# Performance work log

Hardware: AMD Instinct MI355X
Metric: run time of the kernel (lower is better)

The kernel has to match this reference:

```python
import jax, jax.numpy as jnp
import numpy as np

L, H, NH, I = 12, 768, 12, 3072
DH = H // NH
EPS = 1e-12
STD = 0.02

def _ln(x, g, b):
    m = jnp.mean(x, axis=-1, keepdims=True)
    v = jnp.mean(jnp.square(x - m), axis=-1, keepdims=True)
    return (x - m) * jax.lax.rsqrt(v + EPS) * g + b

def setup_inputs() -> dict:
    key = jax.random.key(0)
    ks = jax.random.split(key, 6)
    return {
        "hidden_states": jax.random.normal(ks[0], (8, 512, H), dtype=jnp.float32),
        "attention_mask": jnp.zeros((8, 1, 1, 512), dtype=jnp.float32),
        "normA_gamma": jnp.ones((L, H), jnp.float32),
        "normA_beta": jnp.zeros((L, H), jnp.float32),
        "normB_gamma": jnp.ones((L, H), jnp.float32),
        "normB_beta": jnp.zeros((L, H), jnp.float32),
        "wa": jax.random.normal(ks[1], (L, 3 * H, H), jnp.float32) * STD,
        "ba": jnp.zeros((L, 3 * H), jnp.float32),
        "wb": jax.random.normal(ks[2], (L, H, H), jnp.float32) * STD,
        "bb": jnp.zeros((L, H), jnp.float32),
        "wc": jax.random.normal(ks[3], (L, I, H), jnp.float32) * STD,
        "bc": jnp.zeros((L, I), jnp.float32),
        "wd": jax.random.normal(ks[4], (L, H, I), jnp.float32) * STD,
        "bd": jnp.zeros((L, H), jnp.float32),
    }

def _encoder(hidden_states, attention_mask, normA_gamma, normA_beta, normB_gamma,
             normB_beta, wa, ba, wb, bb, wc, bc, wd, bd):
    B, S, _ = hidden_states.shape
    scale = 1.0 / jnp.sqrt(jnp.float32(DH))

    def layer(x, p):
        ga, bA, gB, bB_, Wa, Ba, Wb, Bb, Wc, Bc, Wd, Bd = p
        # fused QKV: [B,S,3H]
        qkv = jnp.einsum('bsh,oh->bso', x, Wa) + Ba
        q, k, v = jnp.split(qkv, 3, axis=-1)
        q = q.reshape(B, S, NH, DH)
        k = k.reshape(B, S, NH, DH)
        v = v.reshape(B, S, NH, DH)
        scores = jnp.einsum('bqnd,bknd->bnqk', q, k) * scale + attention_mask
        probs = jax.nn.softmax(scores, axis=-1)
        ctx = jnp.einsum('bnqk,bknd->bqnd', probs, v).reshape(B, S, H)
        attn_out = jnp.einsum('bsh,oh->bso', ctx, Wb) + Bb
        x = _ln(x + attn_out, ga, bA)           # post-LN after attention
        h = jax.nn.gelu(jnp.einsum('bsh,ih->bsi', x, Wc) + Bc, approximate=False)
        ffn_out = jnp.einsum('bsi,hi->bsh', h, Wd) + Bd
        x = _ln(x + ffn_out, gB, bB_)           # post-LN after FFN
        return x, None

    params = (normA_gamma, normA_beta, normB_gamma, normB_beta,
              wa, ba, wb, bb, wc, bc, wd, bd)
    out, _ = jax.lax.scan(layer, hidden_states, params)
    return out

def reference(hidden_states, attention_mask, normA_gamma, normA_beta, normB_gamma,
              normB_beta, wa, ba, wb, bb, wc, bc, wd, bd):
    return _encoder(hidden_states, attention_mask, normA_gamma, normA_beta,
                    normB_gamma, normB_beta, wa, ba, wb, bb, wc, bc, wd, bd)
```

## Files before the change

kernel.cpp:

```cpp
#include <hip/hip_runtime.h>
#include <hip/hip_bf16.h>
#include <cmath>

typedef __bf16 bf16;
typedef __attribute__((ext_vector_type(8))) __bf16 bf16x8;
typedef __attribute__((ext_vector_type(4))) float f32x4;
typedef __attribute__((ext_vector_type(8))) short s16x8;

#define DEV __device__ __forceinline__

constexpr int HDIM = 768, NHEADS = 12, DHEAD = 64, IDIM = 3072, BATCH = 8, SEQ = 512;
constexpr int MTOK = BATCH * SEQ;
constexpr int H3 = 3 * HDIM;
constexpr float SCALE = 0.125f;

DEV void gld16(const bf16* g, bf16* l) {
  __builtin_amdgcn_global_load_lds((const __attribute__((address_space(1))) void*)g,
                                   (__attribute__((address_space(3))) void*)l, 16, 0, 0);
}

__global__ void k_cvt(const float* __restrict__ s, bf16* __restrict__ o, long n8) {
  long i = (long)blockIdx.x * blockDim.x + threadIdx.x;
  long st = (long)gridDim.x * blockDim.x;
  for (; i < n8; i += st) {
    const float4* p = (const float4*)s + i * 2;
    float4 v0 = p[0], v1 = p[1];
    union { bf16 t[8]; s16x8 v; } u;
    u.t[0] = (bf16)v0.x; u.t[1] = (bf16)v0.y; u.t[2] = (bf16)v0.z; u.t[3] = (bf16)v0.w;
    u.t[4] = (bf16)v1.x; u.t[5] = (bf16)v1.y; u.t[6] = (bf16)v1.z; u.t[7] = (bf16)v1.w;
    *(s16x8*)(o + i * 8) = u.v;
  }
}

__global__ void k_init_xb(const float* __restrict__ s, bf16* __restrict__ xb, long n8) {
  long i = (long)blockIdx.x * blockDim.x + threadIdx.x;
  long st = (long)gridDim.x * blockDim.x;
  for (; i < n8; i += st) {
    const float4* p = (const float4*)s + i * 2;
    float4 v0 = p[0], v1 = p[1];
    union { bf16 t[8]; s16x8 v; } u;
    u.t[0] = (bf16)v0.x; u.t[1] = (bf16)v0.y; u.t[2] = (bf16)v0.z; u.t[3] = (bf16)v0.w;
    u.t[4] = (bf16)v1.x; u.t[5] = (bf16)v1.y; u.t[6] = (bf16)v1.z; u.t[7] = (bf16)v1.w;
    *(s16x8*)(xb + i * 8) = u.v;
  }
}

template <int OUT>
__global__ __launch_bounds__(256) void k_gemm(const bf16* __restrict__ A,
                                              const bf16* __restrict__ W,
                                              const float* __restrict__ bias,
                                              void* __restrict__ C,
                                              bf16* __restrict__ vt,
                                              int M, int N, int K) {
  __shared__ alignas(128) bf16 As[2][128 * 32];
  __shared__ alignas(128) bf16 Bs[2][128 * 32];
  const int tid = threadIdx.x;
  const int lane = tid & 63, wave = tid >> 6;
  const int wr = wave >> 1, wc = wave & 1;
  const int bx = blockIdx.x, by = blockIdx.y;
  const bf16* Ab = A + (size_t)by * 128 * K;
  const bf16* Bb = W + (size_t)bx * 128 * K;
  const int s0 = tid, s1 = tid + 256;
  const int r0 = s0 >> 2, c0 = ((s0 & 3) ^ ((r0 >> 1) & 3)) << 3;
  const int r1 = s1 >> 2, c1 = ((s1 & 3) ^ ((r1 >> 1) & 3)) << 3;

  f32x4 acc[4][4] = {};
  const int KT = K >> 5;
  int cur = 0;
  gld16(Ab + (size_t)r0 * K + c0, &As[0][s0 * 8]);
  gld16(Ab + (size_t)r1 * K + c1, &As[0][s1 * 8]);
  gld16(Bb + (size_t)r0 * K + c0, &Bs[0][s0 * 8]);
  gld16(Bb + (size_t)r1 * K + c1, &Bs[0][s1 * 8]);

  const int r = lane & 15, kg = lane >> 4;
  for (int kt = 0; kt < KT; ++kt) {
    __syncthreads();
    if (kt + 1 < KT) {
      int k0 = (kt + 1) << 5;
      gld16(Ab + (size_t)r0 * K + k0 + c0, &As[cur ^ 1][s0 * 8]);
      gld16(Ab + (size_t)r1 * K + k0 + c1, &As[cur ^ 1][s1 * 8]);
      gld16(Bb + (size_t)r0 * K + k0 + c0, &Bs[cur ^ 1][s0 * 8]);
      gld16(Bb + (size_t)r1 * K + k0 + c1, &Bs[cur ^ 1][s1 * 8]);
    }
    const bf16* Ac = As[cur];
    const bf16* Bc = Bs[cur];
    bf16x8 af[4], bfr[4];
#pragma unroll
    for (int m = 0; m < 4; ++m) {
      int row = wr * 64 + m * 16 + r;
      af[m] = *(const bf16x8*)(Ac + row * 32 + ((kg ^ ((row >> 1) & 3)) << 3));
    }
#pragma unroll
    for (int n = 0; n < 4; ++n) {
      int row = wc * 64 + n * 16 + r;
      bfr[n] = *(const bf16x8*)(Bc + row * 32 + ((kg ^ ((row >> 1) & 3)) << 3));
    }
#pragma unroll
    for (int m = 0; m < 4; ++m)
#pragma unroll
      for (int n = 0; n < 4; ++n)
        acc[m][n] = __builtin_amdgcn_mfma_f32_16x16x32_bf16(af[m], bfr[n], acc[m][n], 0, 0, 0);
    cur ^= 1;
  }
  const int g = lane >> 4, c16 = lane & 15;
#pragma unroll
  for (int m = 0; m < 4; ++m) {
#pragma unroll
    for (int n = 0; n < 4; ++n) {
      int col = bx * 128 + wc * 64 + n * 16 + c16;
      float bv = bias[col];
      if (OUT == 3 && col >= 2 * HDIM) {
        int hh = (col - 2 * HDIM) >> 6, dd = (col - 2 * HDIM) & 63;
        int row0 = by * 128 + wr * 64 + m * 16 + g * 4;
        int bb_ = row0 >> 9, ss = row0 & 511;
        union { bf16 t[4]; short4 q; } u;
#pragma unroll
        for (int j = 0; j < 4; ++j) u.t[j] = (bf16)(acc[m][n][j] + bv);
        *(short4*)(vt + (((size_t)(bb_ * NHEADS + hh) * DHEAD + dd) * SEQ + ss)) = u.q;
      } else {
#pragma unroll
        for (int j = 0; j < 4; ++j) {
          int row = by * 128 + wr * 64 + m * 16 + g * 4 + j;
          float v = acc[m][n][j] + bv;
          if (OUT == 2) v = 0.5f * v * (1.0f + erff(v * 0.70710678118f));
          ((bf16*)C)[(size_t)row * N + col] = (bf16)v;
        }
      }
    }
  }
}

__global__ __launch_bounds__(256) void k_gemm_sk(const bf16* __restrict__ A,
                                                 const bf16* __restrict__ W,
                                                 bf16* __restrict__ C,
                                                 int M, int N, int Kc, int ld) {
  __shared__ alignas(128) bf16 As[2][128 * 32];
  __shared__ alignas(128) bf16 Bs[2][128 * 32];
  const int tid = threadIdx.x;
  const int lane = tid & 63, wave = tid >> 6;
  const int wr = wave >> 1, wc = wave & 1;
  const int bx = blockIdx.x, by = blockIdx.y, kz = blockIdx.z;
  const bf16* Ab = A + (size_t)by * 128 * ld + (size_t)kz * Kc;
  const bf16* Bb = W + (size_t)bx * 128 * ld + (size_t)kz * Kc;
  bf16* Cz = C + (size_t)kz * M * N;
  const int s0 = tid, s1 = tid + 256;
  const int r0 = s0 >> 2, c0 = ((s0 & 3) ^ ((r0 >> 1) & 3)) << 3;
  const int r1 = s1 >> 2, c1 = ((s1 & 3) ^ ((r1 >> 1) & 3)) << 3;

  f32x4 acc[4][4] = {};
  const int KT = Kc >> 5;
  int cur = 0;
  gld16(Ab + (size_t)r0 * ld + c0, &As[0][s0 * 8]);
  gld16(Ab + (size_t)r1 * ld + c1, &As[0][s1 * 8]);
  gld16(Bb + (size_t)r0 * ld + c0, &Bs[0][s0 * 8]);
  gld16(Bb + (size_t)r1 * ld + c1, &Bs[0][s1 * 8]);

  const int r = lane & 15, kg = lane >> 4;
  for (int kt = 0; kt < KT; ++kt) {
    __syncthreads();
    if (kt + 1 < KT) {
      int k0 = (kt + 1) << 5;
      gld16(Ab + (size_t)r0 * ld + k0 + c0, &As[cur ^ 1][s0 * 8]);
      gld16(Ab + (size_t)r1 * ld + k0 + c1, &As[cur ^ 1][s1 * 8]);
      gld16(Bb + (size_t)r0 * ld + k0 + c0, &Bs[cur ^ 1][s0 * 8]);
      gld16(Bb + (size_t)r1 * ld + k0 + c1, &Bs[cur ^ 1][s1 * 8]);
    }
    const bf16* Ac = As[cur];
    const bf16* Bc = Bs[cur];
    bf16x8 af[4], bfr[4];
#pragma unroll
    for (int m = 0; m < 4; ++m) {
      int row = wr * 64 + m * 16 + r;
      af[m] = *(const bf16x8*)(Ac + row * 32 + ((kg ^ ((row >> 1) & 3)) << 3));
    }
#pragma unroll
    for (int n = 0; n < 4; ++n) {
      int row = wc * 64 + n * 16 + r;
      bfr[n] = *(const bf16x8*)(Bc + row * 32 + ((kg ^ ((row >> 1) & 3)) << 3));
    }
#pragma unroll
    for (int m = 0; m < 4; ++m)
#pragma unroll
      for (int n = 0; n < 4; ++n)
        acc[m][n] = __builtin_amdgcn_mfma_f32_16x16x32_bf16(af[m], bfr[n], acc[m][n], 0, 0, 0);
    cur ^= 1;
  }
  const int g = lane >> 4, c16 = lane & 15;
#pragma unroll
  for (int m = 0; m < 4; ++m)
#pragma unroll
    for (int n = 0; n < 4; ++n) {
      int col = bx * 128 + wc * 64 + n * 16 + c16;
#pragma unroll
      for (int j = 0; j < 4; ++j) {
        int row = by * 128 + wr * 64 + m * 16 + g * 4 + j;
        Cz[(size_t)row * N + col] = (bf16)acc[m][n][j];
      }
    }
}

__global__ __launch_bounds__(256) void k_attn(const bf16* __restrict__ qkv,
                                              const bf16* __restrict__ vT,
                                              const float* __restrict__ mask,
                                              bf16* __restrict__ ctx) {
  __shared__ alignas(128) bf16 smem[20480];
  bf16* Qs = smem;
  bf16* Ks = smem + 4096;
  bf16* Vs = smem;
  bf16* Ps = smem + 16384;
  const int tid = threadIdx.x, lane = tid & 63, wave = tid >> 6;
  const int q0 = blockIdx.x * 64;
  const int h = blockIdx.y, b = blockIdx.z;
  const int bh = b * NHEADS + h;
  const bf16* qbase = qkv + (size_t)(b * SEQ) * H3 + h * DHEAD;
  const bf16* kbase = qbase + HDIM;
  const bf16* Vsrc = vT + (size_t)bh * DHEAD * SEQ;
  const int r15 = lane & 15, kg = lane >> 4;

  for (int s = tid; s < 512; s += 256) {
    int r = s >> 3, sl = s & 7;
    gld16(qbase + (size_t)(q0 + r) * H3 + ((sl ^ (r & 7)) << 3), &Qs[s * 8]);
  }
  f32x4 acc[32];
#pragma unroll
  for (int f = 0; f < 32; ++f) acc[f] = (f32x4){0.f, 0.f, 0.f, 0.f};

  for (int half = 0; half < 2; ++half) {
    for (int s = tid; s < 2048; s += 256) {
      int r = s >> 3, sl = s & 7;
      gld16(kbase + (size_t)(half * 256 + r) * H3 + ((sl ^ (r & 7)) << 3), &Ks[s * 8]);
    }
    __syncthreads();
#pragma unroll
    for (int ks = 0; ks < 2; ++ks) {
      int qrow = wave * 16 + r15;
      int sl = ks * 4 + kg;
      bf16x8 aq = *(const bf16x8*)(Qs + qrow * 64 + ((sl ^ (qrow & 7)) << 3));
#pragma unroll
      for (int nf = 0; nf < 16; ++nf) {
        int krow = nf * 16 + r15;
        bf16x8 bk = *(const bf16x8*)(Ks + krow * 64 + ((sl ^ (krow & 7)) << 3));
        acc[half * 16 + nf] =
            __builtin_amdgcn_mfma_f32_16x16x32_bf16(aq, bk, acc[half * 16 + nf], 0, 0, 0);
      }
    }
    __syncthreads();
  }

#pragma unroll
  for (int i = 0; i < 8; ++i) {
    int g16 = tid + i * 256;
    int d = g16 >> 5, c = g16 & 31;
    gld16(Vsrc + (size_t)d * SEQ + ((c ^ (d & 7)) << 3), &Vs[g16 * 8]);
  }

  const float* mrow = mask + b * SEQ;
#pragma unroll
  for (int f = 0; f < 32; ++f) {
    float mv = mrow[f * 16 + r15];
#pragma unroll
    for (int j = 0; j < 4; ++j) acc[f][j] = acc[f][j] * SCALE + mv;
  }
#pragma unroll
  for (int j = 0; j < 4; ++j) {
    float m = -1e30f;
#pragma unroll
    for (int f = 0; f < 32; ++f) m = fmaxf(m, acc[f][j]);
    m = fmaxf(m, __shfl_xor(m, 1));
    m = fmaxf(m, __shfl_xor(m, 2));
    m = fmaxf(m, __shfl_xor(m, 4));
    m = fmaxf(m, __shfl_xor(m, 8));
    float sum = 0.f;
#pragma unroll
    for (int f = 0; f < 32; ++f) { acc[f][j] = __expf(acc[f][j] - m); sum += acc[f][j]; }
    sum += __shfl_xor(sum, 1);
    sum += __shfl_xor(sum, 2);
    sum += __shfl_xor(sum, 4);
    sum += __shfl_xor(sum, 8);
    float inv = 1.0f / sum;
#pragma unroll
    for (int f = 0; f < 32; ++f) acc[f][j] *= inv;
  }
  __syncthreads();

  f32x4 pvacc[4] = {};
  bf16* Pw = Ps + wave * (16 * 32);
#pragma unroll
  for (int half = 0; half < 2; ++half) {
    if (half == 1) {
      __syncthreads();
#pragma unroll
      for (int i = 0; i < 8; ++i) {
        int g16 = tid + i * 256;
        int d = g16 >> 5, c = g16 & 31;
        gld16(Vsrc + (size_t)d * SEQ + 256 + ((c ^ (d & 7)) << 3), &Vs[g16 * 8]);
      }
      __syncthreads();
    }
#pragma unroll
    for (int kc8 = 0; kc8 < 8; ++kc8) {
      int kc = half * 8 + kc8;
#pragma unroll
      for (int fb = 0; fb < 2; ++fb)
#pragma unroll
        for (int j = 0; j < 4; ++j) {
          int q = kg * 4 + j, k = fb * 16 + r15;
          Pw[q * 32 + ((((k >> 3) ^ ((q >> 1) & 3)) << 3) | (k & 7))] =
              (bf16)acc[kc * 2 + fb][j];
        }
      bf16x8 pa = *(const bf16x8*)(Pw + r15 * 32 + ((kg ^ ((r15 >> 1) & 3)) << 3));
#pragma unroll
      for (int n = 0; n < 4; ++n) {
        int d = n * 16 + r15;
        bf16x8 vb = *(const bf16x8*)(Vs + d * 256 + (((kc8 * 4 + kg) ^ (d & 7)) << 3));
        pvacc[n] = __builtin_amdgcn_mfma_f32_16x16x32_bf16(pa, vb, pvacc[n], 0, 0, 0);
      }
    }
  }

  bf16* crow = ctx + (size_t)(b * SEQ + q0 + wave * 16) * HDIM + h * DHEAD;
#pragma unroll
  for (int n = 0; n < 4; ++n)
#pragma unroll
    for (int j = 0; j < 4; ++j)
      crow[(size_t)(kg * 4 + j) * HDIM + n * 16 + r15] = (bf16)pvacc[n][j];
}

__global__ __launch_bounds__(192) void k_ln4(const bf16* __restrict__ x,
                                             const bf16* __restrict__ d,
                                             const float* __restrict__ bias,
                                             const float* __restrict__ gamma,
                                             const float* __restrict__ beta,
                                             bf16* __restrict__ xo, float* __restrict__ fo) {
  const size_t MH = (size_t)MTOK * HDIM;
  int row = blockIdx.x;
  int t = threadIdx.x;
  int c = t * 4;
  const bf16* xr = x + (size_t)row * HDIM;
  const bf16* dr = d + (size_t)row * HDIM;
  union S4 { bf16 t[4]; short4 s; };
  S4 xv, d0, d1, d2, d3;
  xv.s = *(const short4*)(xr + c);
  d0.s = *(const short4*)(dr + c);
  d1.s = *(const short4*)(dr + MH + c);
  d2.s = *(const short4*)(dr + 2 * MH + c);
  d3.s = *(const short4*)(dr + 3 * MH + c);
  float4 bv = *(const float4*)(bias + c);
  float a[4];
  float s1 = 0.f, s2 = 0.f;
#pragma unroll
  for (int j = 0; j < 4; ++j) {
    float b_ = (j == 0) ? bv.x : (j == 1) ? bv.y : (j == 2) ? bv.z : bv.w;
    a[j] = (float)xv.t[j] + b_ + (float)d0.t[j] + (float)d1.t[j] + (float)d2.t[j] +
           (float)d3.t[j];
    s1 += a[j]; s2 += a[j] * a[j];
  }
#pragma unroll
  for (int o = 32; o; o >>= 1) { s1 += __shfl_down(s1, o); s2 += __shfl_down(s2, o); }
  __shared__ float red[6];
  int wv = t >> 6, lane = t & 63;
  if (lane == 0) { red[wv] = s1; red[3 + wv] = s2; }
  __syncthreads();
  s1 = red[0] + red[1] + red[2];
  s2 = red[3] + red[4] + red[5];
  float mean = s1 * (1.0f / 768.0f);
  float var = s2 * (1.0f / 768.0f) - mean * mean;
  float rs = rsqrtf(var + 1e-12f);
  float4 gv = *(const float4*)(gamma + c);
  float4 btv = *(const float4*)(beta + c);
  float o0 = (a[0] - mean) * rs * gv.x + btv.x;
  float o1 = (a[1] - mean) * rs * gv.y + btv.y;
  float o2 = (a[2] - mean) * rs * gv.z + btv.z;
  float o3 = (a[3] - mean) * rs * gv.w + btv.w;
  S4 ov;
  ov.t[0] = (bf16)o0; ov.t[1] = (bf16)o1; ov.t[2] = (bf16)o2; ov.t[3] = (bf16)o3;
  *(short4*)(xo + (size_t)row * HDIM + c) = ov.s;
  if (fo) {
    float4 f4 = {o0, o1, o2, o3};
    *(float4*)(fo + (size_t)row * HDIM + c) = f4;
  }
}

extern "C" void kernel_launch(void* const* d_in, const int* in_sizes, int n_in,
                              void* d_out, int out_size, void* d_ws, size_t ws_size,
                              hipStream_t stream) {
  const float* hidden = (const float*)d_in[0];
  const float* mask   = (const float*)d_in[1];
  const float* nAg    = (const float*)d_in[2];
  const float* nAb    = (const float*)d_in[3];
  const float* nBg    = (const float*)d_in[4];
  const float* nBb    = (const float*)d_in[5];
  const float* wa     = (const float*)d_in[6];
  const float* ba     = (const float*)d_in[7];
  const float* wb     = (const float*)d_in[8];
  const float* bb     = (const float*)d_in[9];
  const float* wc     = (const float*)d_in[10];
  const float* bc     = (const float*)d_in[11];
  const float* wd     = (const float*)d_in[12];
  const float* bd     = (const float*)d_in[13];

  char* p = (char*)d_ws;
  auto alloc = [&](size_t bytes) {
    char* r = p;
    p += (bytes + 255) & ~(size_t)255;
    return (void*)r;
  };
  bf16* xb    = (bf16*)alloc((size_t)MTOK * HDIM * 2);
  bf16* qkv   = (bf16*)alloc((size_t)MTOK * H3 * 2);
  bf16* vT    = (bf16*)alloc((size_t)BATCH * NHEADS * DHEAD * SEQ * 2);
  bf16* ctx   = (bf16*)alloc((size_t)MTOK * HDIM * 2);
  bf16* hbuf  = (bf16*)alloc((size_t)MTOK * IDIM * 2);
  bf16* dres  = (bf16*)alloc((size_t)4 * MTOK * HDIM * 2);

  const size_t wa_n = (size_t)12 * H3 * HDIM;
  const size_t wb_n = (size_t)12 * HDIM * HDIM;
  const size_t wc_n = (size_t)12 * IDIM * HDIM;
  const size_t wd_n = (size_t)12 * HDIM * IDIM;
  size_t used = (size_t)(p - (char*)d_ws);
  const bool upfront = ws_size >= used + (wa_n + wb_n + wc_n + wd_n) * 2 + 8192;

  bf16* wab = (bf16*)alloc((upfront ? wa_n : (size_t)H3 * HDIM) * 2);
  bf16* wbb = (bf16*)alloc((upfront ? wb_n : (size_t)HDIM * HDIM) * 2);
  bf16* wcb = (bf16*)alloc((upfront ? wc_n : (size_t)IDIM * HDIM) * 2);
  bf16* wdb = (bf16*)alloc((upfront ? wd_n : (size_t)HDIM * IDIM) * 2);

  k_init_xb<<<1024, 256, 0, stream>>>(hidden, xb, (long)MTOK * HDIM / 8);
  if (upfront) {
    k_cvt<<<2048, 256, 0, stream>>>(wa, wab, (long)(wa_n / 8));
    k_cvt<<<2048, 256, 0, stream>>>(wb, wbb, (long)(wb_n / 8));
    k_cvt<<<2048, 256, 0, stream>>>(wc, wcb, (long)(wc_n / 8));
    k_cvt<<<2048, 256, 0, stream>>>(wd, wdb, (long)(wd_n / 8));
  }

  for (int l = 0; l < 12; ++l) {
    bf16* waL = upfront ? wab + (size_t)l * H3 * HDIM : wab;
    bf16* wbL = upfront ? wbb + (size_t)l * HDIM * HDIM : wbb;
    bf16* wcL = upfront ? wcb + (size_t)l * IDIM * HDIM : wcb;
    bf16* wdL = upfront ? wdb + (size_t)l * HDIM * IDIM : wdb;
    if (!upfront) {
      k_cvt<<<2048, 256, 0, stream>>>(wa + (size_t)l * H3 * HDIM, waL, (long)(H3 * HDIM / 8));
      k_cvt<<<2048, 256, 0, stream>>>(wb + (size_t)l * HDIM * HDIM, wbL, (long)(HDIM * HDIM / 8));
      k_cvt<<<2048, 256, 0, stream>>>(wc + (size_t)l * IDIM * HDIM, wcL, (long)(IDIM * HDIM / 8));
      k_cvt<<<2048, 256, 0, stream>>>(wd + (size_t)l * HDIM * IDIM, wdL, (long)(HDIM * IDIM / 8));
    }

    k_gemm<3><<<dim3(H3 / 128, MTOK / 128), 256, 0, stream>>>(
        xb, waL, ba + (size_t)l * H3, qkv, vT, MTOK, H3, HDIM);
    k_attn<<<dim3(SEQ / 64, NHEADS, BATCH), 256, 0, stream>>>(qkv, vT, mask, ctx);
    k_gemm_sk<<<dim3(HDIM / 128, MTOK / 128, 4), 256, 0, stream>>>(
        ctx, wbL, dres, MTOK, HDIM, HDIM / 4, HDIM);
    k_ln4<<<MTOK, 192, 0, stream>>>(xb, dres, bb + (size_t)l * HDIM,
                                    nAg + (size_t)l * HDIM, nAb + (size_t)l * HDIM,
                                    xb, nullptr);
    k_gemm<2><<<dim3(IDIM / 128, MTOK / 128), 256, 0, stream>>>(
        xb, wcL, bc + (size_t)l * IDIM, hbuf, nullptr, MTOK, IDIM, HDIM);
    k_gemm_sk<<<dim3(HDIM / 128, MTOK / 128, 4), 256, 0, stream>>>(
        hbuf, wdL, dres, MTOK, HDIM, IDIM / 4, IDIM);
    k_ln4<<<MTOK, 192, 0, stream>>>(xb, dres, bd + (size_t)l * HDIM,
                                    nBg + (size_t)l * HDIM, nBb + (size_t)l * HDIM,
                                    xb, (l == 11) ? (float*)d_out : nullptr);
  }
}
```

Measured before the change: 2.067 ms.

## Add XCD-aware block swizzle to GEMMs and attention; halve split-K for out-proj

Remaps linear workgroup IDs so consecutive logical tiles land on the same XCD, so blocks that share A/B tiles or the same attention head reuse that XCD's L2. The attention output projection now uses a 2-way split-K instead of 4-way, and the LayerNorm kernel is templated on the number of partial sums. The aim is less L2 thrash across chiplets and less partial-sum traffic for the small GEMM. In exchange the out-projection grid is smaller, leaving fewer blocks to occupy the GPU.

```diff
diff --git a/kernel.cpp b/kernel.cpp
--- a/kernel.cpp
+++ b/kernel.cpp
@@ -45,7 +45,13 @@
   }
 }
 
-template <int OUT>
+template <int NWG>
+DEV int xcd_swz(int id) {
+  static_assert(NWG % 8 == 0, "bijective swizzle needs nwg %% 8 == 0");
+  return (id & 7) * (NWG / 8) + (id >> 3);
+}
+
+template <int OUT, int GX, int GY>
 __global__ __launch_bounds__(256) void k_gemm(const bf16* __restrict__ A,
                                               const bf16* __restrict__ W,
                                               const float* __restrict__ bias,
@@ -57,7 +63,8 @@
   const int tid = threadIdx.x;
   const int lane = tid & 63, wave = tid >> 6;
   const int wr = wave >> 1, wc = wave & 1;
-  const int bx = blockIdx.x, by = blockIdx.y;
+  int id = xcd_swz<GX * GY>(blockIdx.x + GX * blockIdx.y);
+  const int bx = id % GX, by = id / GX;
   const bf16* Ab = A + (size_t)by * 128 * K;
   const bf16* Bb = W + (size_t)bx * 128 * K;
   const int s0 = tid, s1 = tid + 256;
@@ -130,6 +137,7 @@
   }
 }
 
+template <int GX, int GY, int GZ>
 __global__ __launch_bounds__(256) void k_gemm_sk(const bf16* __restrict__ A,
                                                  const bf16* __restrict__ W,
                                                  bf16* __restrict__ C,
@@ -139,7 +147,10 @@
   const int tid = threadIdx.x;
   const int lane = tid & 63, wave = tid >> 6;
   const int wr = wave >> 1, wc = wave & 1;
-  const int bx = blockIdx.x, by = blockIdx.y, kz = blockIdx.z;
+  int id = xcd_swz<GX * GY * GZ>(blockIdx.x + GX * (blockIdx.y + GY * blockIdx.z));
+  const int bx = id % GX;
+  const int t2 = id / GX;
+  const int by = t2 % GY, kz = t2 / GY;
   const bf16* Ab = A + (size_t)by * 128 * ld + (size_t)kz * Kc;
   const bf16* Bb = W + (size_t)bx * 128 * ld + (size_t)kz * Kc;
   bf16* Cz = C + (size_t)kz * M * N;
@@ -209,8 +220,9 @@
   bf16* Vs = smem;
   bf16* Ps = smem + 16384;
   const int tid = threadIdx.x, lane = tid & 63, wave = tid >> 6;
-  const int q0 = blockIdx.x * 64;
-  const int h = blockIdx.y, b = blockIdx.z;
+  int id = xcd_swz<768>(blockIdx.x + 8 * (blockIdx.y + 12 * blockIdx.z));
+  const int q0 = (id & 7) * 64;
+  const int h = (id >> 3) % 12, b = id / 96;
   const int bh = b * NHEADS + h;
   const bf16* qbase = qkv + (size_t)(b * SEQ) * H3 + h * DHEAD;
   const bf16* kbase = qbase + HDIM;
@@ -326,6 +338,7 @@
       crow[(size_t)(kg * 4 + j) * HDIM + n * 16 + r15] = (bf16)pvacc[n][j];
 }
 
+template <int NP>
 __global__ __launch_bounds__(192) void k_ln4(const bf16* __restrict__ x,
                                              const bf16* __restrict__ d,
                                              const float* __restrict__ bias,
@@ -339,20 +352,19 @@
   const bf16* xr = x + (size_t)row * HDIM;
   const bf16* dr = d + (size_t)row * HDIM;
   union S4 { bf16 t[4]; short4 s; };
-  S4 xv, d0, d1, d2, d3;
+  S4 xv, dp[NP];
   xv.s = *(const short4*)(xr + c);
-  d0.s = *(const short4*)(dr + c);
-  d1.s = *(const short4*)(dr + MH + c);
-  d2.s = *(const short4*)(dr + 2 * MH + c);
-  d3.s = *(const short4*)(dr + 3 * MH + c);
+#pragma unroll
+  for (int z = 0; z < NP; ++z) dp[z].s = *(const short4*)(dr + z * MH + c);
   float4 bv = *(const float4*)(bias + c);
   float a[4];
   float s1 = 0.f, s2 = 0.f;
 #pragma unroll
   for (int j = 0; j < 4; ++j) {
     float b_ = (j == 0) ? bv.x : (j == 1) ? bv.y : (j == 2) ? bv.z : bv.w;
-    a[j] = (float)xv.t[j] + b_ + (float)d0.t[j] + (float)d1.t[j] + (float)d2.t[j] +
-           (float)d3.t[j];
+    a[j] = (float)xv.t[j] + b_;
+#pragma unroll
+    for (int z = 0; z < NP; ++z) a[j] += (float)dp[z].t[j];
     s1 += a[j]; s2 += a[j] * a[j];
   }
 #pragma unroll
@@ -444,20 +456,20 @@
       k_cvt<<<2048, 256, 0, stream>>>(wd + (size_t)l * HDIM * IDIM, wdL, (long)(HDIM * IDIM / 8));
     }
 
-    k_gemm<3><<<dim3(H3 / 128, MTOK / 128), 256, 0, stream>>>(
+    k_gemm<3, 18, 32><<<dim3(18, 32), 256, 0, stream>>>(
         xb, waL, ba + (size_t)l * H3, qkv, vT, MTOK, H3, HDIM);
-    k_attn<<<dim3(SEQ / 64, NHEADS, BATCH), 256, 0, stream>>>(qkv, vT, mask, ctx);
-    k_gemm_sk<<<dim3(HDIM / 128, MTOK / 128, 4), 256, 0, stream>>>(
-        ctx, wbL, dres, MTOK, HDIM, HDIM / 4, HDIM);
-    k_ln4<<<MTOK, 192, 0, stream>>>(xb, dres, bb + (size_t)l * HDIM,
-                                    nAg + (size_t)l * HDIM, nAb + (size_t)l * HDIM,
-                                    xb, nullptr);
-    k_gemm<2><<<dim3(IDIM / 128, MTOK / 128), 256, 0, stream>>>(
+    k_attn<<<dim3(8, 12, 8), 256, 0, stream>>>(qkv, vT, mask, ctx);
+    k_gemm_sk<6, 32, 2><<<dim3(6, 32, 2), 256, 0, stream>>>(
+        ctx, wbL, dres, MTOK, HDIM, HDIM / 2, HDIM);
+    k_ln4<2><<<MTOK, 192, 0, stream>>>(xb, dres, bb + (size_t)l * HDIM,
+                                       nAg + (size_t)l * HDIM, nAb + (size_t)l * HDIM,
+                                       xb, nullptr);
+    k_gemm<2, 24, 32><<<dim3(24, 32), 256, 0, stream>>>(
         xb, wcL, bc + (size_t)l * IDIM, hbuf, nullptr, MTOK, IDIM, HDIM);
-    k_gemm_sk<<<dim3(HDIM / 128, MTOK / 128, 4), 256, 0, stream>>>(
+    k_gemm_sk<6, 32, 4><<<dim3(6, 32, 4), 256, 0, stream>>>(
         hbuf, wdL, dres, MTOK, HDIM, IDIM / 4, IDIM);
-    k_ln4<<<MTOK, 192, 0, stream>>>(xb, dres, bd + (size_t)l * HDIM,
-                                    nBg + (size_t)l * HDIM, nBb + (size_t)l * HDIM,
-                                    xb, (l == 11) ? (float*)d_out : nullptr);
-  }
-}
+    k_ln4<4><<<MTOK, 192, 0, stream>>>(xb, dres, bd + (size_t)l * HDIM,
+                                       nBg + (size_t)l * HDIM, nBb + (size_t)l * HDIM,
+                                       xb, (l == 11) ? (float*)d_out : nullptr);
+  }
+}
```

Result: faster. 1.900 ms (-8.1%).
